# Optimization experiments

Hardware: AMD Instinct MI355X
Metric: run time of the kernel (lower is better)

The kernel has to match this reference:

```python
import jax, jax.numpy as jnp
import numpy as np

D_MODEL = 1024
N_EXPERTS = 8
TOP_K = 2
CAP_FACTOR = 1.0
HIDDEN = 2816  # multiple_of*ceil(int(2*4*d/3)/multiple_of) with multiple_of=256


def setup_inputs() -> dict:
    key = jax.random.key(0)
    ks = jax.random.split(key, 8)
    B, S = 2, 2048
    s = 0.02
    return {
        "x": jax.random.normal(ks[0], (B, S, D_MODEL), jnp.float32),
        "noise": jax.random.normal(ks[1], (B, S, N_EXPERTS), jnp.float32),
        "router_w": jax.random.normal(ks[2], (N_EXPERTS, D_MODEL), jnp.float32) * s,
        "router_b": jnp.zeros((N_EXPERTS,), jnp.float32),
        "noise_w": jax.random.normal(ks[3], (N_EXPERTS, D_MODEL), jnp.float32) * s,
        "noise_b": jnp.zeros((N_EXPERTS,), jnp.float32),
        "w1": jax.random.normal(ks[4], (N_EXPERTS, HIDDEN, D_MODEL), jnp.float32) * s,
        "w3": jax.random.normal(ks[5], (N_EXPERTS, HIDDEN, D_MODEL), jnp.float32) * s,
        "w2": jax.random.normal(ks[6], (N_EXPERTS, D_MODEL, HIDDEN), jnp.float32) * s,
    }


def reference(x, noise, router_w, router_b, noise_w, noise_b, w1, w3, w2):
    B, S, d = x.shape
    N = B * S
    capacity = int(N * TOP_K / N_EXPERTS * CAP_FACTOR)
    flat_x = x.reshape(N, d)

    # noisy top-k router
    logits = flat_x @ router_w.T + router_b                      # [N, E]
    noise_logits = flat_x @ noise_w.T + noise_b                  # [N, E]
    noisy = logits + noise.reshape(N, N_EXPERTS) * jax.nn.softplus(noise_logits)
    topv, topi = jax.lax.top_k(noisy, TOP_K)                     # [N, k]
    # softmax over sparse (-inf filled) logits == softmax over top-k values
    gw = jax.nn.softmax(topv, axis=-1)                           # [N, k]

    updates = jnp.zeros_like(flat_x)
    tok_ids = jnp.arange(N, dtype=jnp.int32)
    for e in range(N_EXPERTS):
        hit = topi == e                                          # [N, k]
        gate = jnp.sum(gw * hit, axis=-1)                        # [N]
        m = jnp.any(hit, axis=-1)                                # token routed to e
        pos = jnp.cumsum(m.astype(jnp.int32)) - 1                # rank in flat order
        keep = m & (pos < capacity)                              # capacity truncation (first-come)
        slot = jnp.where(keep, pos, capacity)                    # dropped tokens -> overflow slot
        # gather tokens into fixed-capacity buffer (slot `capacity` is a trash slot)
        buf = jnp.zeros((capacity + 1, d), x.dtype).at[slot].set(flat_x)
        tok = jnp.full((capacity + 1,), N, jnp.int32).at[slot].set(tok_ids)
        xb = buf[:capacity]
        # SwiGLU FFN: w2( silu(x w1^T) * (x w3^T) )
        h = jax.nn.silu(xb @ w1[e].T) * (xb @ w3[e].T)           # [cap, H]
        o = h @ w2[e].T                                          # [cap, d]
        tke = tok[:capacity]
        g = jnp.where(tke < N, gate[jnp.clip(tke, 0, N - 1)], 0.0)
        # scatter-combine; index N drops (empty slots)
        updates = updates.at[tke].add(o * g[:, None], mode="drop")
    return updates.reshape(B, S, d)
```

## Files before the change

kernel.cpp:

```cpp
#include <hip/hip_runtime.h>


#define D_MODEL 1024
#define HIDDEN 2816
#define N_TOK 4096
#define CAP 1024

typedef __attribute__((ext_vector_type(8))) short short8;
typedef __attribute__((ext_vector_type(4))) float f32x4;

__device__ __forceinline__ unsigned short f2bf(float f) {
  unsigned int u = __float_as_uint(f);
  u += 0x7fffu + ((u >> 16) & 1u);
  return (unsigned short)(u >> 16);
}
__device__ __forceinline__ float bf2f(unsigned short h) {
  return __uint_as_float(((unsigned int)h) << 16);
}

template <int Ncnt> __device__ __forceinline__ void waitv() {
  if constexpr (Ncnt == 8)      asm volatile("s_waitcnt vmcnt(8)" ::: "memory");
  else if constexpr (Ncnt == 6) asm volatile("s_waitcnt vmcnt(6)" ::: "memory");
  else                          asm volatile("s_waitcnt vmcnt(0)" ::: "memory");
}

__global__ void router_kernel(const float* __restrict__ x, const float* __restrict__ noise,
                              const float* __restrict__ rw, const float* __restrict__ rb,
                              const float* __restrict__ nw, const float* __restrict__ nb,
                              int* __restrict__ topi, float* __restrict__ gall,
                              int* __restrict__ slot) {
  int wid = threadIdx.x >> 6;
  int lane = threadIdx.x & 63;
  int t = blockIdx.x * 4 + wid;
  if (t >= N_TOK) return;
  const float* xr = x + (size_t)t * D_MODEL;
  double accL[8] = {0,0,0,0,0,0,0,0};
  double accN[8] = {0,0,0,0,0,0,0,0};
  for (int i = 0; i < 4; ++i) {
    int kb = (i * 64 + lane) * 4;
    float4 xv = *(const float4*)(xr + kb);
#pragma unroll
    for (int e = 0; e < 8; ++e) {
      float4 wv = *(const float4*)(rw + e * D_MODEL + kb);
      accL[e] += (double)xv.x * wv.x + (double)xv.y * wv.y + (double)xv.z * wv.z + (double)xv.w * wv.w;
      float4 nv = *(const float4*)(nw + e * D_MODEL + kb);
      accN[e] += (double)xv.x * nv.x + (double)xv.y * nv.y + (double)xv.z * nv.z + (double)xv.w * nv.w;
    }
  }
#pragma unroll
  for (int e = 0; e < 8; ++e) {
    for (int s = 32; s > 0; s >>= 1) {
      accL[e] += __shfl_xor(accL[e], s);
      accN[e] += __shfl_xor(accN[e], s);
    }
  }
  if (lane == 0) {
    double noisy[8];
#pragma unroll
    for (int e = 0; e < 8; ++e) {
      double lg = accL[e] + (double)rb[e];
      double nl = accN[e] + (double)nb[e];
      double sp = (nl > 0.0 ? nl : 0.0) + log1p(exp(-fabs(nl)));
      noisy[e] = lg + (double)noise[t * 8 + e] * sp;
    }
    int i0 = 0;
    for (int e = 1; e < 8; ++e) if (noisy[e] > noisy[i0]) i0 = e;
    int i1 = -1;
    for (int e = 0; e < 8; ++e) { if (e == i0) continue; if (i1 < 0 || noisy[e] > noisy[i1]) i1 = e; }
    double g0 = 1.0 / (1.0 + exp(noisy[i1] - noisy[i0]));
    topi[t * 2] = i0; topi[t * 2 + 1] = i1;
    gall[t * 2] = (float)g0; gall[t * 2 + 1] = (float)(1.0 - g0);
    slot[t * 2] = -1; slot[t * 2 + 1] = -1;
  }
}

__global__ void scan_kernel(const int* __restrict__ topi,
                            int* __restrict__ slot, int* __restrict__ tok_list) {
  int e = blockIdx.x;
  int tid = threadIdx.x;
  int lane = tid & 63, wid = tid >> 6;
  __shared__ int wsum[16];
  __shared__ int base_s;
  tok_list[e * CAP + tid] = -1;
  if (tid == 0) base_s = 0;
  __syncthreads();
  for (int chunk = 0; chunk < N_TOK / 1024; ++chunk) {
    int t = chunk * 1024 + tid;
    int i0 = topi[t * 2], i1 = topi[t * 2 + 1];
    bool m = (i0 == e) || (i1 == e);
    unsigned long long mask = __ballot(m);
    int excl = __popcll(mask & ((1ull << lane) - 1ull));
    if (lane == 0) wsum[wid] = __popcll(mask);
    __syncthreads();
    int base = base_s;
    int woff = 0;
    for (int w = 0; w < wid; ++w) woff += wsum[w];
    int pos = base + woff + excl;
    if (m && pos < CAP) {
      tok_list[e * CAP + pos] = t;
      if (i0 == e) slot[t * 2] = pos; else slot[t * 2 + 1] = pos;
    }
    __syncthreads();
    if (tid == 0) {
      int s = 0;
      for (int w = 0; w < 16; ++w) s += wsum[w];
      base_s = base + s;
    }
    __syncthreads();
  }
}

__global__ void gather_kernel(const float* __restrict__ x, const int* __restrict__ tok_list,
                              unsigned short* __restrict__ xb) {
  int row = blockIdx.x;
  int tok = tok_list[row];
  unsigned short* dst = xb + (size_t)row * D_MODEL + threadIdx.x * 4;
  if (tok < 0) {
    *(ushort4*)dst = make_ushort4(0, 0, 0, 0);
  } else {
    float4 v = *(const float4*)(x + (size_t)tok * D_MODEL + threadIdx.x * 4);
    *(ushort4*)dst = make_ushort4(f2bf(v.x), f2bf(v.y), f2bf(v.z), f2bf(v.w));
  }
}

__global__ void cvt_kernel(const float* __restrict__ src, unsigned short* __restrict__ dst, int n4) {
  int i = blockIdx.x * blockDim.x + threadIdx.x;
  if (i >= n4) return;
  float4 v = *(const float4*)(src + (size_t)i * 4);
  *(ushort4*)(dst + (size_t)i * 4) = make_ushort4(f2bf(v.x), f2bf(v.y), f2bf(v.z), f2bf(v.w));
}

template <int N, int K, int BN, bool CBF16, bool TWO>
__global__ __launch_bounds__(512, 2)
void gemm256(const unsigned short* __restrict__ Ab, const unsigned short* __restrict__ B0,
             const unsigned short* __restrict__ B1, void* __restrict__ C0, void* __restrict__ C1) {
  constexpr int NF = BN / 64;
  constexpr int BUFSZ = 32768 + BN * 128;
  constexpr int ACH = 32;
  constexpr int CH = ACH + BN / 8;
  constexpr int CPW = CH / 8;
  constexpr int KT = K / 64;
  constexpr int NBN = N / BN;
  constexpr int ZDIM = TWO ? 16 : 8;
  constexpr int PERZ = NBN * 4;
  constexpr int NWG = PERZ * ZDIM;

  __shared__ char smem[2 * BUFSZ];

  int lid = blockIdx.x;
  int swz = (lid & 7) * (NWG / 8) + (lid >> 3);
  int z = swz / PERZ;
  int rem = swz - z * PERZ;
  int bm = rem / NBN;
  int bn = rem - bm * NBN;
  int e, which;
  if constexpr (TWO) { e = z >> 1; which = z & 1; } else { e = z; which = 0; }

  const unsigned short* A = Ab + (size_t)e * CAP * K;
  const unsigned short* B = ((TWO && which) ? B1 : B0) + (size_t)e * N * K;
  void* Cp = (TWO && which) ? C1 : C0;

  int tid = threadIdx.x, lane = tid & 63, wid = tid >> 6;
  int wr = wid >> 2, wc = wid & 3;
  int lane15 = lane & 15, lhi = lane >> 4, l7 = lane & 7;

  int lrow = lane >> 3;
  int lcol = ((lane & 7) ^ lrow) * 8;
  const unsigned short* Abase = A + (size_t)(bm * 256 + lrow) * K + lcol;
  const unsigned short* Bbase = B + (size_t)(bn * BN + lrow) * K + lcol;

  auto STAGE = [&](int ktile, int buf) {
    char* lb = smem + buf * BUFSZ;
#pragma unroll
    for (int i = 0; i < CPW; ++i) {
      int c = wid * CPW + i;
      if (c < ACH) {
        const unsigned short* g = Abase + (size_t)(c * 8) * K + ktile * 64;
        __builtin_amdgcn_global_load_lds((const __attribute__((address_space(1))) void*)g,
                                         (__attribute__((address_space(3))) void*)(lb + c * 1024), 16, 0, 0);
      } else {
        int cb = c - ACH;
        const unsigned short* g = Bbase + (size_t)(cb * 8) * K + ktile * 64;
        __builtin_amdgcn_global_load_lds((const __attribute__((address_space(1))) void*)g,
                                         (__attribute__((address_space(3))) void*)(lb + 32768 + cb * 1024), 16, 0, 0);
      }
    }
  };

  int sw0 = ((0 + lhi) ^ l7) * 16;
  int sw1 = ((4 + lhi) ^ l7) * 16;
  int aoff0 = wr * 16384 + lane15 * 128 + sw0;
  int aoff1 = wr * 16384 + lane15 * 128 + sw1;
  int boff0 = 32768 + (wc * (BN / 4) + lane15) * 128 + sw0;
  int boff1 = 32768 + (wc * (BN / 4) + lane15) * 128 + sw1;

  f32x4 acc[8][NF] = {};

  STAGE(0, 0);
  STAGE(1, 1);
  if constexpr (CPW == 8) waitv<8>(); else waitv<6>();
  __builtin_amdgcn_sched_barrier(0);
  __builtin_amdgcn_s_barrier();
  __builtin_amdgcn_sched_barrier(0);

  for (int kt = 0; kt < KT; ++kt) {
    char* cb = smem + (kt & 1) * BUFSZ;
    short8 a0[8], b0[NF], a1[8], b1[NF];
#pragma unroll
    for (int n = 0; n < NF; ++n) b0[n] = *(const short8*)(cb + boff0 + n * 2048);
#pragma unroll
    for (int m = 0; m < 8; ++m) a0[m] = *(const short8*)(cb + aoff0 + m * 2048);
    __builtin_amdgcn_s_setprio(1);
#pragma unroll
    for (int m = 0; m < 8; ++m)
#pragma unroll
      for (int n = 0; n < NF; ++n)
        acc[m][n] = __builtin_amdgcn_mfma_f32_16x16x32_bf16(a0[m], b0[n], acc[m][n], 0, 0, 0);
    __builtin_amdgcn_s_setprio(0);
#pragma unroll
    for (int n = 0; n < NF; ++n) b1[n] = *(const short8*)(cb + boff1 + n * 2048);
#pragma unroll
    for (int m = 0; m < 8; ++m) a1[m] = *(const short8*)(cb + aoff1 + m * 2048);
    asm volatile("" ::: "memory");
    __builtin_amdgcn_sched_barrier(0);
    __builtin_amdgcn_s_barrier();
    __builtin_amdgcn_sched_barrier(0);
    if (kt + 2 < KT) STAGE(kt + 2, kt & 1);
    __builtin_amdgcn_s_setprio(1);
#pragma unroll
    for (int m = 0; m < 8; ++m)
#pragma unroll
      for (int n = 0; n < NF; ++n)
        acc[m][n] = __builtin_amdgcn_mfma_f32_16x16x32_bf16(a1[m], b1[n], acc[m][n], 0, 0, 0);
    __builtin_amdgcn_s_setprio(0);
    if (kt + 2 < KT) { if constexpr (CPW == 8) waitv<8>(); else waitv<6>(); }
    else if (kt + 1 < KT) waitv<0>();
    __builtin_amdgcn_sched_barrier(0);
    if (kt + 1 < KT) __builtin_amdgcn_s_barrier();
    __builtin_amdgcn_sched_barrier(0);
  }

  size_t cbase = (size_t)e * CAP * N;
#pragma unroll
  for (int m = 0; m < 8; ++m) {
#pragma unroll
    for (int n = 0; n < NF; ++n) {
      int row0 = bm * 256 + wr * 128 + m * 16 + lhi * 4;
      int col = bn * BN + wc * (BN / 4) + n * 16 + lane15;
#pragma unroll
      for (int j = 0; j < 4; ++j) {
        size_t idx = cbase + (size_t)(row0 + j) * N + col;
        if constexpr (CBF16) ((unsigned short*)Cp)[idx] = f2bf(acc[m][n][j]);
        else                 ((float*)Cp)[idx] = acc[m][n][j];
      }
    }
  }
}

__global__ void silu_kernel(unsigned short* __restrict__ h1, const unsigned short* __restrict__ h3,
                            int n4) {
  int i = blockIdx.x * blockDim.x + threadIdx.x;
  if (i >= n4) return;
  ushort4 a = *(const ushort4*)(h1 + (size_t)i * 4);
  ushort4 b = *(const ushort4*)(h3 + (size_t)i * 4);
  float av[4] = {bf2f(a.x), bf2f(a.y), bf2f(a.z), bf2f(a.w)};
  float bv[4] = {bf2f(b.x), bf2f(b.y), bf2f(b.z), bf2f(b.w)};
  unsigned short r[4];
#pragma unroll
  for (int j = 0; j < 4; ++j) {
    float s = av[j] / (1.0f + __expf(-av[j])) * bv[j];
    r[j] = f2bf(s);
  }
  *(ushort4*)(h1 + (size_t)i * 4) = make_ushort4(r[0], r[1], r[2], r[3]);
}

__global__ void combine_kernel(const float* __restrict__ o, const int* __restrict__ topi,
                               const float* __restrict__ gall, const int* __restrict__ slot,
                               float* __restrict__ out) {
  int t = blockIdx.x;
  int d = threadIdx.x * 4;
  int i0 = topi[t * 2], i1 = topi[t * 2 + 1];
  int s0 = slot[t * 2], s1 = slot[t * 2 + 1];
  float g0 = gall[t * 2], g1 = gall[t * 2 + 1];
  float4 r = make_float4(0.f, 0.f, 0.f, 0.f);
  if (s0 >= 0) {
    float4 v = *(const float4*)(o + ((size_t)i0 * CAP + s0) * D_MODEL + d);
    r.x += g0 * v.x; r.y += g0 * v.y; r.z += g0 * v.z; r.w += g0 * v.w;
  }
  if (s1 >= 0) {
    float4 v = *(const float4*)(o + ((size_t)i1 * CAP + s1) * D_MODEL + d);
    r.x += g1 * v.x; r.y += g1 * v.y; r.z += g1 * v.z; r.w += g1 * v.w;
  }
  *(float4*)(out + (size_t)t * D_MODEL + d) = r;
}

extern "C" void kernel_launch(void* const* d_in, const int* in_sizes, int n_in,
                              void* d_out, int out_size, void* d_ws, size_t ws_size,
                              hipStream_t stream) {
  const float* x     = (const float*)d_in[0];
  const float* noise = (const float*)d_in[1];
  const float* rw    = (const float*)d_in[2];
  const float* rb    = (const float*)d_in[3];
  const float* nw    = (const float*)d_in[4];
  const float* nb    = (const float*)d_in[5];
  const float* w1    = (const float*)d_in[6];
  const float* w3    = (const float*)d_in[7];
  const float* w2    = (const float*)d_in[8];
  float* out = (float*)d_out;

  char* ws = (char*)d_ws;
  size_t off = 0;
  auto alloc = [&](size_t bytes) -> void* {
    void* p = ws + off;
    off += (bytes + 255) & ~(size_t)255;
    return p;
  };
  const size_t WELEM = (size_t)8 * HIDDEN * D_MODEL;
  unsigned short* wb1 = (unsigned short*)alloc(WELEM * 2);
  unsigned short* wb3 = (unsigned short*)alloc(WELEM * 2);
  unsigned short* wb2 = (unsigned short*)alloc(WELEM * 2);
  unsigned short* xb  = (unsigned short*)alloc((size_t)8 * CAP * D_MODEL * 2);
  unsigned short* h1  = (unsigned short*)alloc((size_t)8 * CAP * HIDDEN * 2);
  unsigned short* h3  = (unsigned short*)alloc((size_t)8 * CAP * HIDDEN * 2);
  float*          ob  = (float*)alloc((size_t)8 * CAP * D_MODEL * 4);
  int*   topi = (int*)alloc(N_TOK * 2 * 4);
  float* gall = (float*)alloc(N_TOK * 2 * 4);
  int*   slot = (int*)alloc(N_TOK * 2 * 4);
  int*   tokl = (int*)alloc(8 * CAP * 4);
  (void)ws_size; (void)in_sizes; (void)n_in; (void)out_size;

  const int n4w = (int)(WELEM / 4);
  cvt_kernel<<<(n4w + 255) / 256, 256, 0, stream>>>(w1, wb1, n4w);
  cvt_kernel<<<(n4w + 255) / 256, 256, 0, stream>>>(w3, wb3, n4w);
  cvt_kernel<<<(n4w + 255) / 256, 256, 0, stream>>>(w2, wb2, n4w);

  router_kernel<<<N_TOK / 4, 256, 0, stream>>>(x, noise, rw, rb, nw, nb, topi, gall, slot);
  scan_kernel<<<8, 1024, 0, stream>>>(topi, slot, tokl);
  gather_kernel<<<8 * CAP, 256, 0, stream>>>(x, tokl, xb);

  gemm256<HIDDEN, D_MODEL, 256, true, true><<<dim3(704), 512, 0, stream>>>(
      xb, wb1, wb3, (void*)h1, (void*)h3);

  const int n4h = (int)((size_t)8 * CAP * HIDDEN / 4);
  silu_kernel<<<(n4h + 255) / 256, 256, 0, stream>>>(h1, h3, n4h);

  gemm256<D_MODEL, HIDDEN, 128, false, false><<<dim3(256), 512, 0, stream>>>(
      h1, wb2, nullptr, (void*)ob, nullptr);

  combine_kernel<<<N_TOK, 256, 0, stream>>>(ob, topi, gall, slot, out);
}
```

Before: 353.1 us.

## Fuse fp32 weight conversion into GEMM loads and SiLU-gate into first GEMM epilogue

Removes the separate weight fp32-to-bf16 conversion kernels. Each GEMM now loads fp32 weights into registers, converts them, and writes bf16 into LDS, software-pipelined two tiles ahead. The first GEMM computes the w1 and w3 tiles together and applies SiLU times gate in its epilogue, which drops the h3 buffer and the silu kernel. This saves the weight round-trip and intermediate traffic but doubles weight load bytes per tile in the GEMM and raises register pressure.

```diff
diff --git a/kernel.cpp b/kernel.cpp
--- a/kernel.cpp
+++ b/kernel.cpp
@@ -19,8 +19,9 @@
 }
 
 template <int Ncnt> __device__ __forceinline__ void waitv() {
-  if constexpr (Ncnt == 8)      asm volatile("s_waitcnt vmcnt(8)" ::: "memory");
-  else if constexpr (Ncnt == 6) asm volatile("s_waitcnt vmcnt(6)" ::: "memory");
+  if constexpr (Ncnt == 12)     asm volatile("s_waitcnt vmcnt(12)" ::: "memory");
+  else if constexpr (Ncnt == 8) asm volatile("s_waitcnt vmcnt(8)" ::: "memory");
+  else if constexpr (Ncnt == 4) asm volatile("s_waitcnt vmcnt(4)" ::: "memory");
   else                          asm volatile("s_waitcnt vmcnt(0)" ::: "memory");
 }
 
@@ -123,43 +124,29 @@
   }
 }
 
-__global__ void cvt_kernel(const float* __restrict__ src, unsigned short* __restrict__ dst, int n4) {
-  int i = blockIdx.x * blockDim.x + threadIdx.x;
-  if (i >= n4) return;
-  float4 v = *(const float4*)(src + (size_t)i * 4);
-  *(ushort4*)(dst + (size_t)i * 4) = make_ushort4(f2bf(v.x), f2bf(v.y), f2bf(v.z), f2bf(v.w));
-}
-
-template <int N, int K, int BN, bool CBF16, bool TWO>
+template <int N, int K, int NW, bool FUSE>
 __global__ __launch_bounds__(512, 2)
-void gemm256(const unsigned short* __restrict__ Ab, const unsigned short* __restrict__ B0,
-             const unsigned short* __restrict__ B1, void* __restrict__ C0, void* __restrict__ C1) {
-  constexpr int NF = BN / 64;
-  constexpr int BUFSZ = 32768 + BN * 128;
-  constexpr int ACH = 32;
-  constexpr int CH = ACH + BN / 8;
-  constexpr int CPW = CH / 8;
+void gemm_fused(const unsigned short* __restrict__ Ab, const float* __restrict__ W0,
+                const float* __restrict__ W1, void* __restrict__ OUT) {
+  constexpr int ABYTES = 32768;
+  constexpr int BBYTES = NW * 16384;
+  constexpr int BUFSZ = ABYTES + BBYTES;
   constexpr int KT = K / 64;
-  constexpr int NBN = N / BN;
-  constexpr int ZDIM = TWO ? 16 : 8;
-  constexpr int PERZ = NBN * 4;
-  constexpr int NWG = PERZ * ZDIM;
+  constexpr int NBN = N / 128;
+  constexpr int NWG = NBN * 4 * 8;
+  constexpr int SL = NW * 2;
+  constexpr int NB = SL * 2;
 
   __shared__ char smem[2 * BUFSZ];
 
   int lid = blockIdx.x;
   int swz = (lid & 7) * (NWG / 8) + (lid >> 3);
-  int z = swz / PERZ;
-  int rem = swz - z * PERZ;
+  int e = swz / (NBN * 4);
+  int rem = swz - e * (NBN * 4);
   int bm = rem / NBN;
   int bn = rem - bm * NBN;
-  int e, which;
-  if constexpr (TWO) { e = z >> 1; which = z & 1; } else { e = z; which = 0; }
 
   const unsigned short* A = Ab + (size_t)e * CAP * K;
-  const unsigned short* B = ((TWO && which) ? B1 : B0) + (size_t)e * N * K;
-  void* Cp = (TWO && which) ? C1 : C0;
-
   int tid = threadIdx.x, lane = tid & 63, wid = tid >> 6;
   int wr = wid >> 2, wc = wid & 3;
   int lane15 = lane & 15, lhi = lane >> 4, l7 = lane & 7;
@@ -167,111 +154,161 @@
   int lrow = lane >> 3;
   int lcol = ((lane & 7) ^ lrow) * 8;
   const unsigned short* Abase = A + (size_t)(bm * 256 + lrow) * K + lcol;
-  const unsigned short* Bbase = B + (size_t)(bn * BN + lrow) * K + lcol;
-
-  auto STAGE = [&](int ktile, int buf) {
+
+  auto ASTAGE = [&](int ktile, int buf) {
     char* lb = smem + buf * BUFSZ;
 #pragma unroll
-    for (int i = 0; i < CPW; ++i) {
-      int c = wid * CPW + i;
-      if (c < ACH) {
-        const unsigned short* g = Abase + (size_t)(c * 8) * K + ktile * 64;
-        __builtin_amdgcn_global_load_lds((const __attribute__((address_space(1))) void*)g,
-                                         (__attribute__((address_space(3))) void*)(lb + c * 1024), 16, 0, 0);
-      } else {
-        int cb = c - ACH;
-        const unsigned short* g = Bbase + (size_t)(cb * 8) * K + ktile * 64;
-        __builtin_amdgcn_global_load_lds((const __attribute__((address_space(1))) void*)g,
-                                         (__attribute__((address_space(3))) void*)(lb + 32768 + cb * 1024), 16, 0, 0);
-      }
+    for (int i = 0; i < 4; ++i) {
+      int c = wid * 4 + i;
+      const unsigned short* g = Abase + (size_t)(c * 8) * K + ktile * 64;
+      __builtin_amdgcn_global_load_lds((const __attribute__((address_space(1))) void*)g,
+                                       (__attribute__((address_space(3))) void*)(lb + c * 1024), 16, 0, 0);
+    }
+  };
+
+  const float* wptr[SL];
+  int woff[SL];
+#pragma unroll
+  for (int i = 0; i < SL; ++i) {
+    int L = i * 512 + tid;
+    int p = (L >> 3) & 127;
+    int ks = L & 7;
+    const float* Wb = ((i >> 1) ? W1 : W0);
+    wptr[i] = Wb + (size_t)e * N * K + (size_t)(bn * 128 + p) * K + ks * 8;
+    woff[i] = ABYTES + (i >> 1) * 16384 + p * 128 + ((ks ^ (p & 7)) * 16);
+  }
+
+  auto BLOAD = [&](int ktile, float4 (&r)[SL][2]) {
+#pragma unroll
+    for (int i = 0; i < SL; ++i) {
+      const float* s = wptr[i] + (size_t)ktile * 64;
+      r[i][0] = *(const float4*)(s);
+      r[i][1] = *(const float4*)(s + 4);
+    }
+  };
+  auto BWRITE = [&](int buf, const float4 (&r)[SL][2]) {
+    char* lb = smem + buf * BUFSZ;
+#pragma unroll
+    for (int i = 0; i < SL; ++i) {
+      short8 v;
+      v[0] = (short)f2bf(r[i][0].x); v[1] = (short)f2bf(r[i][0].y);
+      v[2] = (short)f2bf(r[i][0].z); v[3] = (short)f2bf(r[i][0].w);
+      v[4] = (short)f2bf(r[i][1].x); v[5] = (short)f2bf(r[i][1].y);
+      v[6] = (short)f2bf(r[i][1].z); v[7] = (short)f2bf(r[i][1].w);
+      *(short8*)(lb + woff[i]) = v;
     }
   };
 
   int sw0 = ((0 + lhi) ^ l7) * 16;
   int sw1 = ((4 + lhi) ^ l7) * 16;
-  int aoff0 = wr * 16384 + lane15 * 128 + sw0;
-  int aoff1 = wr * 16384 + lane15 * 128 + sw1;
-  int boff0 = 32768 + (wc * (BN / 4) + lane15) * 128 + sw0;
-  int boff1 = 32768 + (wc * (BN / 4) + lane15) * 128 + sw1;
-
-  f32x4 acc[8][NF] = {};
-
-  STAGE(0, 0);
-  STAGE(1, 1);
-  if constexpr (CPW == 8) waitv<8>(); else waitv<6>();
+
+  f32x4 acc[8][NW][2] = {};
+  float4 rb0[SL][2], rb1[SL][2];
+
+  BLOAD(0, rb0);
+  ASTAGE(0, 0);
+  waitv<4>();
+  BWRITE(0, rb0);
+  BLOAD(1, rb1);
+  ASTAGE(1, 1);
+  waitv<NB + 4>();
+  asm volatile("s_waitcnt lgkmcnt(0)" ::: "memory");
   __builtin_amdgcn_sched_barrier(0);
   __builtin_amdgcn_s_barrier();
   __builtin_amdgcn_sched_barrier(0);
 
-  for (int kt = 0; kt < KT; ++kt) {
+  auto ITER = [&](int kt, float4 (&rLd)[SL][2], float4 (&rWr)[SL][2]) {
     char* cb = smem + (kt & 1) * BUFSZ;
-    short8 a0[8], b0[NF], a1[8], b1[NF];
-#pragma unroll
-    for (int n = 0; n < NF; ++n) b0[n] = *(const short8*)(cb + boff0 + n * 2048);
-#pragma unroll
-    for (int m = 0; m < 8; ++m) a0[m] = *(const short8*)(cb + aoff0 + m * 2048);
+    if (kt + 2 < KT) BLOAD(kt + 2, rLd);
+    short8 a0[8], b0[NW][2], a1[8], b1[NW][2];
+#pragma unroll
+    for (int w = 0; w < NW; ++w)
+#pragma unroll
+      for (int n = 0; n < 2; ++n)
+        b0[w][n] = *(const short8*)(cb + ABYTES + w * 16384 + wc * 4096 + n * 2048 + lane15 * 128 + sw0);
+#pragma unroll
+    for (int m = 0; m < 8; ++m)
+      a0[m] = *(const short8*)(cb + wr * 16384 + m * 2048 + lane15 * 128 + sw0);
     __builtin_amdgcn_s_setprio(1);
 #pragma unroll
     for (int m = 0; m < 8; ++m)
 #pragma unroll
-      for (int n = 0; n < NF; ++n)
-        acc[m][n] = __builtin_amdgcn_mfma_f32_16x16x32_bf16(a0[m], b0[n], acc[m][n], 0, 0, 0);
+      for (int w = 0; w < NW; ++w)
+#pragma unroll
+        for (int n = 0; n < 2; ++n)
+          acc[m][w][n] = __builtin_amdgcn_mfma_f32_16x16x32_bf16(a0[m], b0[w][n], acc[m][w][n], 0, 0, 0);
     __builtin_amdgcn_s_setprio(0);
 #pragma unroll
-    for (int n = 0; n < NF; ++n) b1[n] = *(const short8*)(cb + boff1 + n * 2048);
-#pragma unroll
-    for (int m = 0; m < 8; ++m) a1[m] = *(const short8*)(cb + aoff1 + m * 2048);
-    asm volatile("" ::: "memory");
+    for (int w = 0; w < NW; ++w)
+#pragma unroll
+      for (int n = 0; n < 2; ++n)
+        b1[w][n] = *(const short8*)(cb + ABYTES + w * 16384 + wc * 4096 + n * 2048 + lane15 * 128 + sw1);
+#pragma unroll
+    for (int m = 0; m < 8; ++m)
+      a1[m] = *(const short8*)(cb + wr * 16384 + m * 2048 + lane15 * 128 + sw1);
     __builtin_amdgcn_sched_barrier(0);
     __builtin_amdgcn_s_barrier();
     __builtin_amdgcn_sched_barrier(0);
-    if (kt + 2 < KT) STAGE(kt + 2, kt & 1);
+    if (kt + 1 < KT) {
+      if (kt + 2 < KT) waitv<4 + NB>(); else waitv<4>();
+      BWRITE((kt + 1) & 1, rWr);
+    }
+    if (kt + 2 < KT) ASTAGE(kt + 2, kt & 1);
     __builtin_amdgcn_s_setprio(1);
 #pragma unroll
     for (int m = 0; m < 8; ++m)
 #pragma unroll
-      for (int n = 0; n < NF; ++n)
-        acc[m][n] = __builtin_amdgcn_mfma_f32_16x16x32_bf16(a1[m], b1[n], acc[m][n], 0, 0, 0);
+      for (int w = 0; w < NW; ++w)
+#pragma unroll
+        for (int n = 0; n < 2; ++n)
+          acc[m][w][n] = __builtin_amdgcn_mfma_f32_16x16x32_bf16(a1[m], b1[w][n], acc[m][w][n], 0, 0, 0);
     __builtin_amdgcn_s_setprio(0);
-    if (kt + 2 < KT) { if constexpr (CPW == 8) waitv<8>(); else waitv<6>(); }
-    else if (kt + 1 < KT) waitv<0>();
-    __builtin_amdgcn_sched_barrier(0);
-    if (kt + 1 < KT) __builtin_amdgcn_s_barrier();
-    __builtin_amdgcn_sched_barrier(0);
-  }
-
-  size_t cbase = (size_t)e * CAP * N;
-#pragma unroll
-  for (int m = 0; m < 8; ++m) {
-#pragma unroll
-    for (int n = 0; n < NF; ++n) {
-      int row0 = bm * 256 + wr * 128 + m * 16 + lhi * 4;
-      int col = bn * BN + wc * (BN / 4) + n * 16 + lane15;
-#pragma unroll
-      for (int j = 0; j < 4; ++j) {
-        size_t idx = cbase + (size_t)(row0 + j) * N + col;
-        if constexpr (CBF16) ((unsigned short*)Cp)[idx] = f2bf(acc[m][n][j]);
-        else                 ((float*)Cp)[idx] = acc[m][n][j];
+    if (kt + 1 < KT) {
+      if (kt + 2 < KT) waitv<NB + 4>(); else waitv<0>();
+      asm volatile("s_waitcnt lgkmcnt(0)" ::: "memory");
+      __builtin_amdgcn_sched_barrier(0);
+      __builtin_amdgcn_s_barrier();
+      __builtin_amdgcn_sched_barrier(0);
+    }
+  };
+
+#pragma unroll 1
+  for (int kt2 = 0; kt2 < KT; kt2 += 2) {
+    ITER(kt2, rb0, rb1);
+    ITER(kt2 + 1, rb1, rb0);
+  }
+
+  if constexpr (FUSE) {
+    unsigned short* H = (unsigned short*)OUT + (size_t)e * CAP * N;
+#pragma unroll
+    for (int m = 0; m < 8; ++m) {
+#pragma unroll
+      for (int n = 0; n < 2; ++n) {
+        int row0 = bm * 256 + wr * 128 + m * 16 + lhi * 4;
+        int col = bn * 128 + wc * 32 + n * 16 + lane15;
+#pragma unroll
+        for (int j = 0; j < 4; ++j) {
+          float g1 = acc[m][0][n][j];
+          float g3 = acc[m][NW - 1][n][j];
+          float hv = g1 / (1.0f + __expf(-g1)) * g3;
+          H[(size_t)(row0 + j) * N + col] = f2bf(hv);
+        }
       }
     }
-  }
-}
-
-__global__ void silu_kernel(unsigned short* __restrict__ h1, const unsigned short* __restrict__ h3,
-                            int n4) {
-  int i = blockIdx.x * blockDim.x + threadIdx.x;
-  if (i >= n4) return;
-  ushort4 a = *(const ushort4*)(h1 + (size_t)i * 4);
-  ushort4 b = *(const ushort4*)(h3 + (size_t)i * 4);
-  float av[4] = {bf2f(a.x), bf2f(a.y), bf2f(a.z), bf2f(a.w)};
-  float bv[4] = {bf2f(b.x), bf2f(b.y), bf2f(b.z), bf2f(b.w)};
-  unsigned short r[4];
-#pragma unroll
-  for (int j = 0; j < 4; ++j) {
-    float s = av[j] / (1.0f + __expf(-av[j])) * bv[j];
-    r[j] = f2bf(s);
-  }
-  *(ushort4*)(h1 + (size_t)i * 4) = make_ushort4(r[0], r[1], r[2], r[3]);
+  } else {
+    float* O = (float*)OUT + (size_t)e * CAP * N;
+#pragma unroll
+    for (int m = 0; m < 8; ++m) {
+#pragma unroll
+      for (int n = 0; n < 2; ++n) {
+        int row0 = bm * 256 + wr * 128 + m * 16 + lhi * 4;
+        int col = bn * 128 + wc * 32 + n * 16 + lane15;
+#pragma unroll
+        for (int j = 0; j < 4; ++j)
+          O[(size_t)(row0 + j) * N + col] = acc[m][0][n][j];
+      }
+    }
+  }
 }
 
 __global__ void combine_kernel(const float* __restrict__ o, const int* __restrict__ topi,
@@ -315,37 +352,22 @@
     off += (bytes + 255) & ~(size_t)255;
     return p;
   };
-  const size_t WELEM = (size_t)8 * HIDDEN * D_MODEL;
-  unsigned short* wb1 = (unsigned short*)alloc(WELEM * 2);
-  unsigned short* wb3 = (unsigned short*)alloc(WELEM * 2);
-  unsigned short* wb2 = (unsigned short*)alloc(WELEM * 2);
-  unsigned short* xb  = (unsigned short*)alloc((size_t)8 * CAP * D_MODEL * 2);
-  unsigned short* h1  = (unsigned short*)alloc((size_t)8 * CAP * HIDDEN * 2);
-  unsigned short* h3  = (unsigned short*)alloc((size_t)8 * CAP * HIDDEN * 2);
-  float*          ob  = (float*)alloc((size_t)8 * CAP * D_MODEL * 4);
+  unsigned short* xb = (unsigned short*)alloc((size_t)8 * CAP * D_MODEL * 2);
+  unsigned short* h  = (unsigned short*)alloc((size_t)8 * CAP * HIDDEN * 2);
+  float*          ob = (float*)alloc((size_t)8 * CAP * D_MODEL * 4);
   int*   topi = (int*)alloc(N_TOK * 2 * 4);
   float* gall = (float*)alloc(N_TOK * 2 * 4);
   int*   slot = (int*)alloc(N_TOK * 2 * 4);
   int*   tokl = (int*)alloc(8 * CAP * 4);
   (void)ws_size; (void)in_sizes; (void)n_in; (void)out_size;
 
-  const int n4w = (int)(WELEM / 4);
-  cvt_kernel<<<(n4w + 255) / 256, 256, 0, stream>>>(w1, wb1, n4w);
-  cvt_kernel<<<(n4w + 255) / 256, 256, 0, stream>>>(w3, wb3, n4w);
-  cvt_kernel<<<(n4w + 255) / 256, 256, 0, stream>>>(w2, wb2, n4w);
-
   router_kernel<<<N_TOK / 4, 256, 0, stream>>>(x, noise, rw, rb, nw, nb, topi, gall, slot);
   scan_kernel<<<8, 1024, 0, stream>>>(topi, slot, tokl);
   gather_kernel<<<8 * CAP, 256, 0, stream>>>(x, tokl, xb);
 
-  gemm256<HIDDEN, D_MODEL, 256, true, true><<<dim3(704), 512, 0, stream>>>(
-      xb, wb1, wb3, (void*)h1, (void*)h3);
-
-  const int n4h = (int)((size_t)8 * CAP * HIDDEN / 4);
-  silu_kernel<<<(n4h + 255) / 256, 256, 0, stream>>>(h1, h3, n4h);
-
-  gemm256<D_MODEL, HIDDEN, 128, false, false><<<dim3(256), 512, 0, stream>>>(
-      h1, wb2, nullptr, (void*)ob, nullptr);
+  gemm_fused<HIDDEN, D_MODEL, 2, true><<<dim3(704), 512, 0, stream>>>(xb, w1, w3, (void*)h);
+
+  gemm_fused<D_MODEL, HIDDEN, 1, false><<<dim3(256), 512, 0, stream>>>(h, w2, nullptr, (void*)ob);
 
   combine_kernel<<<N_TOK, 256, 0, stream>>>(ob, topi, gall, slot, out);
 }
```

After: 460.3 us. +30.3%, slower.

## Fuse SiLU-gating into w1/w3 GEMM and gated scatter-combine into w2 GEMM

Applied to the files above, without the earlier changes.

The first GEMM now computes the w1 and w3 tiles together in one workgroup (two B panels per K step) and applies silu(g1)*g3 in the epilogue. This removes the separate h1/h3 round trip through memory and the silu kernel. The second GEMM scatters gate-weighted outputs directly into the zeroed output with atomicAdd, which replaces the fp32 expert-output buffer and the combine kernel. The three weight conversions are merged into one launch. In exchange it adds a memset, float atomics with nondeterministic summation order, and a larger LDS footprint with one workgroup per CU.

```diff
diff --git a/kernel.cpp b/kernel.cpp
--- a/kernel.cpp
+++ b/kernel.cpp
@@ -74,8 +74,9 @@
   }
 }
 
-__global__ void scan_kernel(const int* __restrict__ topi,
-                            int* __restrict__ slot, int* __restrict__ tok_list) {
+__global__ void scan_kernel(const int* __restrict__ topi, const float* __restrict__ gall,
+                            int* __restrict__ slot, int* __restrict__ tok_list,
+                            float* __restrict__ gslot) {
   int e = blockIdx.x;
   int tid = threadIdx.x;
   int lane = tid & 63, wid = tid >> 6;
@@ -98,6 +99,7 @@
     int pos = base + woff + excl;
     if (m && pos < CAP) {
       tok_list[e * CAP + pos] = t;
+      gslot[e * CAP + pos] = gall[t * 2 + (i0 == e ? 0 : 1)];
       if (i0 == e) slot[t * 2] = pos; else slot[t * 2 + 1] = pos;
     }
     __syncthreads();
@@ -123,43 +125,38 @@
   }
 }
 
-__global__ void cvt_kernel(const float* __restrict__ src, unsigned short* __restrict__ dst, int n4) {
+__global__ void cvt3_kernel(const float* __restrict__ s0, const float* __restrict__ s1,
+                            const float* __restrict__ s2, unsigned short* __restrict__ d0,
+                            unsigned short* __restrict__ d1, unsigned short* __restrict__ d2) {
   int i = blockIdx.x * blockDim.x + threadIdx.x;
-  if (i >= n4) return;
+  const float* src = (blockIdx.y == 0) ? s0 : (blockIdx.y == 1) ? s1 : s2;
+  unsigned short* dst = (blockIdx.y == 0) ? d0 : (blockIdx.y == 1) ? d1 : d2;
   float4 v = *(const float4*)(src + (size_t)i * 4);
   *(ushort4*)(dst + (size_t)i * 4) = make_ushort4(f2bf(v.x), f2bf(v.y), f2bf(v.z), f2bf(v.w));
 }
 
-template <int N, int K, int BN, bool CBF16, bool TWO>
-__global__ __launch_bounds__(512, 2)
-void gemm256(const unsigned short* __restrict__ Ab, const unsigned short* __restrict__ B0,
-             const unsigned short* __restrict__ B1, void* __restrict__ C0, void* __restrict__ C1) {
-  constexpr int NF = BN / 64;
-  constexpr int BUFSZ = 32768 + BN * 128;
-  constexpr int ACH = 32;
-  constexpr int CH = ACH + BN / 8;
-  constexpr int CPW = CH / 8;
+template <int NOUT, int K, int NW, int MODE>
+__global__ __launch_bounds__(512, 1)
+void gemm_moe(const unsigned short* __restrict__ Ab, const unsigned short* __restrict__ B0,
+              const unsigned short* __restrict__ B1, void* __restrict__ OUT,
+              const int* __restrict__ tokl, const float* __restrict__ gslot) {
+  constexpr int ABYTES = 32768;
+  constexpr int BUFSZ = ABYTES + NW * 16384;
   constexpr int KT = K / 64;
-  constexpr int NBN = N / BN;
-  constexpr int ZDIM = TWO ? 16 : 8;
-  constexpr int PERZ = NBN * 4;
-  constexpr int NWG = PERZ * ZDIM;
+  constexpr int NBN = NOUT / 128;
+  constexpr int NWG = 8 * 4 * NBN;
+  constexpr int CPW = (32 + NW * 16) / 8;
 
   __shared__ char smem[2 * BUFSZ];
 
   int lid = blockIdx.x;
   int swz = (lid & 7) * (NWG / 8) + (lid >> 3);
-  int z = swz / PERZ;
-  int rem = swz - z * PERZ;
+  int e = swz / (4 * NBN);
+  int rem = swz - e * (4 * NBN);
   int bm = rem / NBN;
   int bn = rem - bm * NBN;
-  int e, which;
-  if constexpr (TWO) { e = z >> 1; which = z & 1; } else { e = z; which = 0; }
 
   const unsigned short* A = Ab + (size_t)e * CAP * K;
-  const unsigned short* B = ((TWO && which) ? B1 : B0) + (size_t)e * N * K;
-  void* Cp = (TWO && which) ? C1 : C0;
-
   int tid = threadIdx.x, lane = tid & 63, wid = tid >> 6;
   int wr = wid >> 2, wc = wid & 3;
   int lane15 = lane & 15, lhi = lane >> 4, l7 = lane & 7;
@@ -167,61 +164,69 @@
   int lrow = lane >> 3;
   int lcol = ((lane & 7) ^ lrow) * 8;
   const unsigned short* Abase = A + (size_t)(bm * 256 + lrow) * K + lcol;
-  const unsigned short* Bbase = B + (size_t)(bn * BN + lrow) * K + lcol;
+  const unsigned short* Bb0 = B0 + (size_t)e * NOUT * K + (size_t)(bn * 128 + lrow) * K + lcol;
+  const unsigned short* Bb1 = (NW == 2)
+      ? B1 + (size_t)e * NOUT * K + (size_t)(bn * 128 + lrow) * K + lcol : Bb0;
 
   auto STAGE = [&](int ktile, int buf) {
     char* lb = smem + buf * BUFSZ;
 #pragma unroll
     for (int i = 0; i < CPW; ++i) {
       int c = wid * CPW + i;
-      if (c < ACH) {
+      if (c < 32) {
         const unsigned short* g = Abase + (size_t)(c * 8) * K + ktile * 64;
         __builtin_amdgcn_global_load_lds((const __attribute__((address_space(1))) void*)g,
                                          (__attribute__((address_space(3))) void*)(lb + c * 1024), 16, 0, 0);
       } else {
-        int cb = c - ACH;
-        const unsigned short* g = Bbase + (size_t)(cb * 8) * K + ktile * 64;
+        int cb2 = c - 32;
+        const unsigned short* base = (cb2 >> 4) ? Bb1 : Bb0;
+        const unsigned short* g = base + (size_t)((cb2 & 15) * 8) * K + ktile * 64;
         __builtin_amdgcn_global_load_lds((const __attribute__((address_space(1))) void*)g,
-                                         (__attribute__((address_space(3))) void*)(lb + 32768 + cb * 1024), 16, 0, 0);
+                                         (__attribute__((address_space(3))) void*)(lb + ABYTES + cb2 * 1024), 16, 0, 0);
       }
     }
   };
 
   int sw0 = ((0 + lhi) ^ l7) * 16;
   int sw1 = ((4 + lhi) ^ l7) * 16;
-  int aoff0 = wr * 16384 + lane15 * 128 + sw0;
-  int aoff1 = wr * 16384 + lane15 * 128 + sw1;
-  int boff0 = 32768 + (wc * (BN / 4) + lane15) * 128 + sw0;
-  int boff1 = 32768 + (wc * (BN / 4) + lane15) * 128 + sw1;
-
-  f32x4 acc[8][NF] = {};
+
+  f32x4 acc[8][NW][2] = {};
 
   STAGE(0, 0);
   STAGE(1, 1);
-  if constexpr (CPW == 8) waitv<8>(); else waitv<6>();
+  waitv<CPW>();
   __builtin_amdgcn_sched_barrier(0);
   __builtin_amdgcn_s_barrier();
   __builtin_amdgcn_sched_barrier(0);
 
   for (int kt = 0; kt < KT; ++kt) {
     char* cb = smem + (kt & 1) * BUFSZ;
-    short8 a0[8], b0[NF], a1[8], b1[NF];
-#pragma unroll
-    for (int n = 0; n < NF; ++n) b0[n] = *(const short8*)(cb + boff0 + n * 2048);
-#pragma unroll
-    for (int m = 0; m < 8; ++m) a0[m] = *(const short8*)(cb + aoff0 + m * 2048);
+    short8 a0[8], b0[NW][2], a1[8], b1[NW][2];
+#pragma unroll
+    for (int w = 0; w < NW; ++w)
+#pragma unroll
+      for (int n = 0; n < 2; ++n)
+        b0[w][n] = *(const short8*)(cb + ABYTES + w * 16384 + wc * 4096 + n * 2048 + lane15 * 128 + sw0);
+#pragma unroll
+    for (int m = 0; m < 8; ++m)
+      a0[m] = *(const short8*)(cb + wr * 16384 + m * 2048 + lane15 * 128 + sw0);
     __builtin_amdgcn_s_setprio(1);
 #pragma unroll
     for (int m = 0; m < 8; ++m)
 #pragma unroll
-      for (int n = 0; n < NF; ++n)
-        acc[m][n] = __builtin_amdgcn_mfma_f32_16x16x32_bf16(a0[m], b0[n], acc[m][n], 0, 0, 0);
+      for (int w = 0; w < NW; ++w)
+#pragma unroll
+        for (int n = 0; n < 2; ++n)
+          acc[m][w][n] = __builtin_amdgcn_mfma_f32_16x16x32_bf16(a0[m], b0[w][n], acc[m][w][n], 0, 0, 0);
     __builtin_amdgcn_s_setprio(0);
 #pragma unroll
-    for (int n = 0; n < NF; ++n) b1[n] = *(const short8*)(cb + boff1 + n * 2048);
-#pragma unroll
-    for (int m = 0; m < 8; ++m) a1[m] = *(const short8*)(cb + aoff1 + m * 2048);
-    asm volatile("" ::: "memory");
+    for (int w = 0; w < NW; ++w)
+#pragma unroll
+      for (int n = 0; n < 2; ++n)
+        b1[w][n] = *(const short8*)(cb + ABYTES + w * 16384 + wc * 4096 + n * 2048 + lane15 * 128 + sw1);
+#pragma unroll
+    for (int m = 0; m < 8; ++m)
+      a1[m] = *(const short8*)(cb + wr * 16384 + m * 2048 + lane15 * 128 + sw1);
     __builtin_amdgcn_sched_barrier(0);
     __builtin_amdgcn_s_barrier();
     __builtin_amdgcn_sched_barrier(0);
@@ -230,68 +235,55 @@
 #pragma unroll
     for (int m = 0; m < 8; ++m)
 #pragma unroll
-      for (int n = 0; n < NF; ++n)
-        acc[m][n] = __builtin_amdgcn_mfma_f32_16x16x32_bf16(a1[m], b1[n], acc[m][n], 0, 0, 0);
+      for (int w = 0; w < NW; ++w)
+#pragma unroll
+        for (int n = 0; n < 2; ++n)
+          acc[m][w][n] = __builtin_amdgcn_mfma_f32_16x16x32_bf16(a1[m], b1[w][n], acc[m][w][n], 0, 0, 0);
     __builtin_amdgcn_s_setprio(0);
-    if (kt + 2 < KT) { if constexpr (CPW == 8) waitv<8>(); else waitv<6>(); }
+    if (kt + 2 < KT) waitv<CPW>();
     else if (kt + 1 < KT) waitv<0>();
     __builtin_amdgcn_sched_barrier(0);
     if (kt + 1 < KT) __builtin_amdgcn_s_barrier();
     __builtin_amdgcn_sched_barrier(0);
   }
 
-  size_t cbase = (size_t)e * CAP * N;
-#pragma unroll
-  for (int m = 0; m < 8; ++m) {
-#pragma unroll
-    for (int n = 0; n < NF; ++n) {
-      int row0 = bm * 256 + wr * 128 + m * 16 + lhi * 4;
-      int col = bn * BN + wc * (BN / 4) + n * 16 + lane15;
-#pragma unroll
-      for (int j = 0; j < 4; ++j) {
-        size_t idx = cbase + (size_t)(row0 + j) * N + col;
-        if constexpr (CBF16) ((unsigned short*)Cp)[idx] = f2bf(acc[m][n][j]);
-        else                 ((float*)Cp)[idx] = acc[m][n][j];
+  if constexpr (MODE == 1) {
+    unsigned short* H = (unsigned short*)OUT + (size_t)e * CAP * NOUT;
+#pragma unroll
+    for (int m = 0; m < 8; ++m) {
+#pragma unroll
+      for (int n = 0; n < 2; ++n) {
+        int row0 = bm * 256 + wr * 128 + m * 16 + lhi * 4;
+        int col = bn * 128 + wc * 32 + n * 16 + lane15;
+#pragma unroll
+        for (int j = 0; j < 4; ++j) {
+          float g1 = acc[m][0][n][j];
+          float g3 = acc[m][1][n][j];
+          float hv = g1 / (1.0f + __expf(-g1)) * g3;
+          H[(size_t)(row0 + j) * NOUT + col] = f2bf(hv);
+        }
       }
     }
-  }
-}
-
-__global__ void silu_kernel(unsigned short* __restrict__ h1, const unsigned short* __restrict__ h3,
-                            int n4) {
-  int i = blockIdx.x * blockDim.x + threadIdx.x;
-  if (i >= n4) return;
-  ushort4 a = *(const ushort4*)(h1 + (size_t)i * 4);
-  ushort4 b = *(const ushort4*)(h3 + (size_t)i * 4);
-  float av[4] = {bf2f(a.x), bf2f(a.y), bf2f(a.z), bf2f(a.w)};
-  float bv[4] = {bf2f(b.x), bf2f(b.y), bf2f(b.z), bf2f(b.w)};
-  unsigned short r[4];
-#pragma unroll
-  for (int j = 0; j < 4; ++j) {
-    float s = av[j] / (1.0f + __expf(-av[j])) * bv[j];
-    r[j] = f2bf(s);
-  }
-  *(ushort4*)(h1 + (size_t)i * 4) = make_ushort4(r[0], r[1], r[2], r[3]);
-}
-
-__global__ void combine_kernel(const float* __restrict__ o, const int* __restrict__ topi,
-                               const float* __restrict__ gall, const int* __restrict__ slot,
-                               float* __restrict__ out) {
-  int t = blockIdx.x;
-  int d = threadIdx.x * 4;
-  int i0 = topi[t * 2], i1 = topi[t * 2 + 1];
-  int s0 = slot[t * 2], s1 = slot[t * 2 + 1];
-  float g0 = gall[t * 2], g1 = gall[t * 2 + 1];
-  float4 r = make_float4(0.f, 0.f, 0.f, 0.f);
-  if (s0 >= 0) {
-    float4 v = *(const float4*)(o + ((size_t)i0 * CAP + s0) * D_MODEL + d);
-    r.x += g0 * v.x; r.y += g0 * v.y; r.z += g0 * v.z; r.w += g0 * v.w;
-  }
-  if (s1 >= 0) {
-    float4 v = *(const float4*)(o + ((size_t)i1 * CAP + s1) * D_MODEL + d);
-    r.x += g1 * v.x; r.y += g1 * v.y; r.z += g1 * v.z; r.w += g1 * v.w;
-  }
-  *(float4*)(out + (size_t)t * D_MODEL + d) = r;
+  } else {
+    float* out = (float*)OUT;
+#pragma unroll
+    for (int m = 0; m < 8; ++m) {
+#pragma unroll
+      for (int n = 0; n < 2; ++n) {
+        int row0 = bm * 256 + wr * 128 + m * 16 + lhi * 4;
+        int col = bn * 128 + wc * 32 + n * 16 + lane15;
+#pragma unroll
+        for (int j = 0; j < 4; ++j) {
+          int gr = e * CAP + row0 + j;
+          int t = tokl[gr];
+          if (t >= 0) {
+            float g = gslot[gr];
+            atomicAdd(out + (size_t)t * D_MODEL + col, g * acc[m][0][n][j]);
+          }
+        }
+      }
+    }
+  }
 }
 
 extern "C" void kernel_launch(void* const* d_in, const int* in_sizes, int n_in,
@@ -320,32 +312,26 @@
   unsigned short* wb3 = (unsigned short*)alloc(WELEM * 2);
   unsigned short* wb2 = (unsigned short*)alloc(WELEM * 2);
   unsigned short* xb  = (unsigned short*)alloc((size_t)8 * CAP * D_MODEL * 2);
-  unsigned short* h1  = (unsigned short*)alloc((size_t)8 * CAP * HIDDEN * 2);
-  unsigned short* h3  = (unsigned short*)alloc((size_t)8 * CAP * HIDDEN * 2);
-  float*          ob  = (float*)alloc((size_t)8 * CAP * D_MODEL * 4);
-  int*   topi = (int*)alloc(N_TOK * 2 * 4);
-  float* gall = (float*)alloc(N_TOK * 2 * 4);
-  int*   slot = (int*)alloc(N_TOK * 2 * 4);
-  int*   tokl = (int*)alloc(8 * CAP * 4);
+  unsigned short* h   = (unsigned short*)alloc((size_t)8 * CAP * HIDDEN * 2);
+  int*   topi  = (int*)alloc(N_TOK * 2 * 4);
+  float* gall  = (float*)alloc(N_TOK * 2 * 4);
+  int*   slot  = (int*)alloc(N_TOK * 2 * 4);
+  int*   tokl  = (int*)alloc(8 * CAP * 4);
+  float* gslot = (float*)alloc(8 * CAP * 4);
   (void)ws_size; (void)in_sizes; (void)n_in; (void)out_size;
 
   const int n4w = (int)(WELEM / 4);
-  cvt_kernel<<<(n4w + 255) / 256, 256, 0, stream>>>(w1, wb1, n4w);
-  cvt_kernel<<<(n4w + 255) / 256, 256, 0, stream>>>(w3, wb3, n4w);
-  cvt_kernel<<<(n4w + 255) / 256, 256, 0, stream>>>(w2, wb2, n4w);
+  cvt3_kernel<<<dim3(n4w / 256, 3), 256, 0, stream>>>(w1, w3, w2, wb1, wb3, wb2);
 
   router_kernel<<<N_TOK / 4, 256, 0, stream>>>(x, noise, rw, rb, nw, nb, topi, gall, slot);
-  scan_kernel<<<8, 1024, 0, stream>>>(topi, slot, tokl);
+  scan_kernel<<<8, 1024, 0, stream>>>(topi, gall, slot, tokl, gslot);
   gather_kernel<<<8 * CAP, 256, 0, stream>>>(x, tokl, xb);
 
-  gemm256<HIDDEN, D_MODEL, 256, true, true><<<dim3(704), 512, 0, stream>>>(
-      xb, wb1, wb3, (void*)h1, (void*)h3);
-
-  const int n4h = (int)((size_t)8 * CAP * HIDDEN / 4);
-  silu_kernel<<<(n4h + 255) / 256, 256, 0, stream>>>(h1, h3, n4h);
-
-  gemm256<D_MODEL, HIDDEN, 128, false, false><<<dim3(256), 512, 0, stream>>>(
-      h1, wb2, nullptr, (void*)ob, nullptr);
-
-  combine_kernel<<<N_TOK, 256, 0, stream>>>(ob, topi, gall, slot, out);
-}
+  hipMemsetAsync(d_out, 0, (size_t)N_TOK * D_MODEL * 4, stream);
+
+  gemm_moe<HIDDEN, D_MODEL, 2, 1><<<dim3(704), 512, 0, stream>>>(
+      xb, wb1, wb3, (void*)h, nullptr, nullptr);
+
+  gemm_moe<D_MODEL, HIDDEN, 1, 2><<<dim3(256), 512, 0, stream>>>(
+      h, wb2, nullptr, (void*)out, tokl, gslot);
+}
```

Result: faster. 332.6 us (-5.8%).
